# Optimization experiments

Measured on AMD Instinct MI355X. Metric: run time of the kernel, lower is better.

The kernel has to match this reference:

```python
import jax, jax.numpy as jnp
import numpy as np

H = W = 20  # module hardcodes visual_feature_map_h/w = 20
STAGES = 6
IN_POINTS = 36
HID = 256
B = 1024


def grid_sample_bilinear_border(fm, grid):
    """PyTorch-equivalent grid_sample, mode='bilinear', padding_mode='border',
    align_corners=False. fm: (B,C,H,W); grid: (B,P,2) in [-1,1] (x,y order).
    Returns (B,C,P)."""
    b, c, h, w = fm.shape
    # unnormalize (align_corners=False), then border-clip the coordinate
    x = jnp.clip((grid[..., 0] + 1.0) * w * 0.5 - 0.5, 0.0, w - 1.0)  # (B,P)
    y = jnp.clip((grid[..., 1] + 1.0) * h * 0.5 - 0.5, 0.0, h - 1.0)
    x0f = jnp.floor(x); y0f = jnp.floor(y)
    wx = (x - x0f)[:, None, :]  # (B,1,P)
    wy = (y - y0f)[:, None, :]
    x0 = x0f.astype(jnp.int32); y0 = y0f.astype(jnp.int32)
    x1 = jnp.minimum(x0 + 1, w - 1); y1 = jnp.minimum(y0 + 1, h - 1)
    fmf = fm.reshape(b, c, h * w)

    def gather(yi, xi):
        idx = (yi * w + xi)[:, None, :]  # (B,1,P)
        return jnp.take_along_axis(fmf, jnp.broadcast_to(idx, (b, c, idx.shape[-1])), axis=2)

    v00 = gather(y0, x0); v01 = gather(y0, x1)
    v10 = gather(y1, x0); v11 = gather(y1, x1)
    return (v00 * (1 - wx) * (1 - wy) + v01 * wx * (1 - wy)
            + v10 * (1 - wx) * wy + v11 * wx * wy)


def setup_inputs() -> dict:
    key = jax.random.key(0)
    ks = jax.random.split(key, 16)
    s = 0.02  # small param scale so sampled points stay mostly in-grid
    return {
        "sampling_query": jax.random.normal(ks[0], (B, HID), jnp.float32),
        "reference_point": jax.random.uniform(ks[1], (B, 2), jnp.float32),
        "feature_map": jax.random.normal(ks[2], (B, HID, H * W), jnp.float32),
        "pos": jax.random.normal(ks[3], (B, HID, H * W), jnp.float32),
        "offset_W": jax.random.normal(ks[4], (STAGES, IN_POINTS * 2, HID), jnp.float32) * s,
        "offset_b": jax.random.uniform(ks[5], (STAGES, IN_POINTS * 2), jnp.float32) - 0.5,
        "up_W1": jax.random.normal(ks[6], (STAGES, HID, 2 * HID), jnp.float32) * s,
        "up_b1": jax.random.normal(ks[7], (STAGES, HID), jnp.float32) * s,
        "up_W2": jax.random.normal(ks[8], (STAGES, HID, HID), jnp.float32) * s,
        "up_b2": jax.random.normal(ks[9], (STAGES, HID), jnp.float32) * s,
        "bbox_W1": jax.random.normal(ks[10], (HID, HID), jnp.float32) * s,
        "bbox_b1": jax.random.normal(ks[11], (HID,), jnp.float32) * s,
        "bbox_W2": jax.random.normal(ks[12], (HID, HID), jnp.float32) * s,
        "bbox_b2": jax.random.normal(ks[13], (HID,), jnp.float32) * s,
        "bbox_W3": jax.random.normal(ks[14], (4, HID), jnp.float32) * s,
        "bbox_b3": jax.random.normal(ks[15], (4,), jnp.float32) * s,
    }


def reference(sampling_query, reference_point, feature_map, pos,
              offset_W, offset_b, up_W1, up_b1, up_W2, up_b2,
              bbox_W1, bbox_b1, bbox_W2, bbox_b2, bbox_W3, bbox_b3):
    bs = sampling_query.shape[0]
    fm = feature_map.reshape(bs, HID, H, W)
    pm = pos.reshape(bs, HID, H, W)
    q = sampling_query
    for s in range(STAGES):  # fixed small stage count -> Python loop ok
        # offset generator: Linear(hidden -> in_points*2)
        xy = (q @ offset_W[s].T + offset_b[s]).reshape(bs, IN_POINTS, 2)
        pts = xy + reference_point[:, None, :]          # (B,P,2) in [0,1]
        grid = 2.0 * pts - 1.0                          # -> [-1,1]
        sampled = grid_sample_bilinear_border(fm, grid)  # (B,C,P)
        pe = grid_sample_bilinear_border(pm, grid)       # (B,C,P)
        fused = (sampled + pe).mean(axis=-1)             # (B,C) pooled over points
        # update_sampling_queries[s]: MLP(2*hidden -> hidden -> hidden)
        cat = jnp.concatenate([fused, q], axis=1)        # (B,2C)
        hdd = jax.nn.relu(cat @ up_W1[s].T + up_b1[s])
        q = hdd @ up_W2[s].T + up_b2[s]
    # bbox_embed: 3-layer MLP, relu on first two, sigmoid box
    hx = jax.nn.relu(q @ bbox_W1.T + bbox_b1)
    hx = jax.nn.relu(hx @ bbox_W2.T + bbox_b2)
    pred_box = jax.nn.sigmoid(hx @ bbox_W3.T + bbox_b3)  # (B,4)
    return pred_box
```

## Files before the change

kernel.cpp:

```cpp
#include <hip/hip_runtime.h>
#include <hip/hip_bf16.h>

#define B_SZ   1024
#define HIDN   256
#define NSTAGE 6
#define NPTS   36
#define HGT    20
#define WID    20
#define HW     400
#define MB     4
#define NTHR   1024

static __device__ __forceinline__ unsigned int f2bf(float x) {
    unsigned int u = __float_as_uint(x);
    u += 0x7FFFu + ((u >> 16) & 1u);
    return u >> 16;
}
static __device__ __forceinline__ float bf2f(unsigned short h) {
    return __uint_as_float((unsigned int)h << 16);
}

__global__ __launch_bounds__(512) void prepass_kernel(
    const float* __restrict__ fm, const float* __restrict__ pos,
    unsigned short* __restrict__ fmp)
{
    const int b  = blockIdx.y;
    const int ct = blockIdx.x;
    __shared__ unsigned short tile[HW * 65];
    const int t = threadIdx.x;

    const size_t gbase = ((size_t)b * HIDN + ct * 64) * HW;
    for (int i = t; i < 6400; i += 512) {
        const int c  = i / 100;
        const int k4 = i - c * 100;
        const float4 a = *(const float4*)(fm  + gbase + 4 * (size_t)i);
        const float4 p = *(const float4*)(pos + gbase + 4 * (size_t)i);
        tile[(4 * k4 + 0) * 65 + c] = (unsigned short)f2bf(a.x + p.x);
        tile[(4 * k4 + 1) * 65 + c] = (unsigned short)f2bf(a.y + p.y);
        tile[(4 * k4 + 2) * 65 + c] = (unsigned short)f2bf(a.z + p.z);
        tile[(4 * k4 + 3) * 65 + c] = (unsigned short)f2bf(a.w + p.w);
    }
    __syncthreads();

    const int u2 = t & 31;
    const int h0 = t >> 5;
    uint* outp = (uint*)(fmp + (((size_t)b * 4 + ct) * HW) * 64);
    for (int hw = h0; hw < HW; hw += 16) {
        const unsigned int lo = tile[hw * 65 + 2 * u2 + 0];
        const unsigned int hi = tile[hw * 65 + 2 * u2 + 1];
        outp[(size_t)hw * 32 + u2] = lo | (hi << 16);
    }
}

template <int K, int O, int ACT>
__device__ __forceinline__ void gemm_v3(
    const float* __restrict__ W, const float* __restrict__ bias,
    const float* __restrict__ i0, const float* __restrict__ i1,
    const float* __restrict__ i2, const float* __restrict__ i3,
    float* __restrict__ o0, float* __restrict__ o1,
    float* __restrict__ o2, float* __restrict__ o3,
    int kp, int og)
{
    const float4* p0 = (const float4*)i0;
    const float4* p1 = (const float4*)i1;
    const float4* p2 = (const float4*)i2;
    const float4* p3 = (const float4*)i3;
    #pragma unroll
    for (int pass = 0; pass < (O + 127) / 128; ++pass) {
        const int o = pass * 128 + og;
        float a0 = 0.f, a1 = 0.f, a2 = 0.f, a3 = 0.f;
        if (o < O) {
            const float4* wr = (const float4*)(W + (size_t)o * K);
            #pragma unroll 4
            for (int jj = 0; jj < K / 32; ++jj) {
                const int j = kp + 8 * jj;
                const float4 w  = wr[j];
                const float4 v0 = p0[j];
                const float4 v1 = p1[j];
                const float4 v2 = p2[j];
                const float4 v3 = p3[j];
                a0 += w.x * v0.x + w.y * v0.y + w.z * v0.z + w.w * v0.w;
                a1 += w.x * v1.x + w.y * v1.y + w.z * v1.z + w.w * v1.w;
                a2 += w.x * v2.x + w.y * v2.y + w.z * v2.z + w.w * v2.w;
                a3 += w.x * v3.x + w.y * v3.y + w.z * v3.z + w.w * v3.w;
            }
        }
        a0 += __shfl_xor(a0, 1); a0 += __shfl_xor(a0, 2); a0 += __shfl_xor(a0, 4);
        a1 += __shfl_xor(a1, 1); a1 += __shfl_xor(a1, 2); a1 += __shfl_xor(a1, 4);
        a2 += __shfl_xor(a2, 1); a2 += __shfl_xor(a2, 2); a2 += __shfl_xor(a2, 4);
        a3 += __shfl_xor(a3, 1); a3 += __shfl_xor(a3, 2); a3 += __shfl_xor(a3, 4);
        if (kp == 0 && o < O) {
            const float bz = bias[o];
            float r0 = a0 + bz, r1 = a1 + bz, r2 = a2 + bz, r3 = a3 + bz;
            if (ACT == 1) {
                r0 = fmaxf(r0, 0.f); r1 = fmaxf(r1, 0.f);
                r2 = fmaxf(r2, 0.f); r3 = fmaxf(r3, 0.f);
            }
            if (ACT == 2) {
                r0 = 1.f / (1.f + expf(-r0)); r1 = 1.f / (1.f + expf(-r1));
                r2 = 1.f / (1.f + expf(-r2)); r3 = 1.f / (1.f + expf(-r3));
            }
            o0[o] = r0; o1[o] = r1; o2[o] = r2; o3[o] = r3;
        }
    }
}

__global__ __launch_bounds__(NTHR) void mdetr5_kernel(
    const float* __restrict__ q_in,  const float* __restrict__ refpt,
    const unsigned short* __restrict__ fmp,
    const float* __restrict__ offW,  const float* __restrict__ offB,
    const float* __restrict__ uW1,   const float* __restrict__ uB1,
    const float* __restrict__ uW2,   const float* __restrict__ uB2,
    const float* __restrict__ bW1,   const float* __restrict__ bb1,
    const float* __restrict__ bW2,   const float* __restrict__ bb2,
    const float* __restrict__ bW3,   const float* __restrict__ bb3,
    float* __restrict__ out)
{
    const int b0 = blockIdx.x * MB;
    const int t  = threadIdx.x;
    const int kp = t & 7;
    const int og = t >> 3;

    __shared__ __attribute__((aligned(16))) float cat_s[MB][2 * HIDN];
    __shared__ __attribute__((aligned(16))) float hdd_s[MB][HIDN];
    __shared__ __attribute__((aligned(16))) float xy_s[MB][80];
    __shared__ __attribute__((aligned(16))) float wgt_s[MB][144];
    __shared__ __attribute__((aligned(16))) int   off_s[MB][144];

    {
        const int m = t >> 8, c = t & 255;
        cat_s[m][HIDN + c] = q_in[(size_t)(b0 + m) * HIDN + c];
    }

    for (int s = 0; s < NSTAGE; ++s) {
        __syncthreads();
        gemm_v3<HIDN, NPTS * 2, 0>(
            offW + (size_t)s * NPTS * 2 * HIDN, offB + s * NPTS * 2,
            cat_s[0] + HIDN, cat_s[1] + HIDN, cat_s[2] + HIDN, cat_s[3] + HIDN,
            xy_s[0], xy_s[1], xy_s[2], xy_s[3], kp, og);
        __syncthreads();
        if (t < MB * NPTS) {
            const int m = t / NPTS, p = t % NPTS;
            const int bm = b0 + m;
            float px = xy_s[m][2 * p + 0] + refpt[2 * bm + 0];
            float py = xy_s[m][2 * p + 1] + refpt[2 * bm + 1];
            float x = fminf(fmaxf(px * (float)WID - 0.5f, 0.f), (float)(WID - 1));
            float y = fminf(fmaxf(py * (float)HGT - 0.5f, 0.f), (float)(HGT - 1));
            float x0f = floorf(x), y0f = floorf(y);
            float wx = x - x0f,   wy = y - y0f;
            int x0 = (int)x0f, y0 = (int)y0f;
            int x1 = min(x0 + 1, WID - 1), y1 = min(y0 + 1, HGT - 1);
            const float inv = 1.f / (float)NPTS;
            wgt_s[m][4 * p + 0] = (1.f - wx) * (1.f - wy) * inv;
            wgt_s[m][4 * p + 1] = wx * (1.f - wy) * inv;
            wgt_s[m][4 * p + 2] = (1.f - wx) * wy * inv;
            wgt_s[m][4 * p + 3] = wx * wy * inv;
            off_s[m][4 * p + 0] = (y0 * WID + x0) * 64;
            off_s[m][4 * p + 1] = (y0 * WID + x1) * 64;
            off_s[m][4 * p + 2] = (y1 * WID + x0) * 64;
            off_s[m][4 * p + 3] = (y1 * WID + x1) * 64;
        }
        __syncthreads();
        {
            const int m = t >> 8, c = t & 255;
            const unsigned short* base =
                fmp + (((size_t)(b0 + m) * 4 + (c >> 6)) * HW) * 64 + (c & 63);
            float acc = 0.f;
            #pragma unroll 6
            for (int p = 0; p < NPTS; ++p) {
                const int4   o4 = ((const int4*)off_s[m])[p];
                const float4 w4 = ((const float4*)wgt_s[m])[p];
                acc += w4.x * bf2f(base[o4.x]) + w4.y * bf2f(base[o4.y])
                     + w4.z * bf2f(base[o4.z]) + w4.w * bf2f(base[o4.w]);
            }
            cat_s[m][c] = acc;
        }
        __syncthreads();
        gemm_v3<2 * HIDN, HIDN, 1>(
            uW1 + (size_t)s * HIDN * 2 * HIDN, uB1 + s * HIDN,
            cat_s[0], cat_s[1], cat_s[2], cat_s[3],
            hdd_s[0], hdd_s[1], hdd_s[2], hdd_s[3], kp, og);
        __syncthreads();
        gemm_v3<HIDN, HIDN, 0>(
            uW2 + (size_t)s * HIDN * HIDN, uB2 + s * HIDN,
            hdd_s[0], hdd_s[1], hdd_s[2], hdd_s[3],
            cat_s[0] + HIDN, cat_s[1] + HIDN, cat_s[2] + HIDN, cat_s[3] + HIDN,
            kp, og);
    }
    __syncthreads();
    gemm_v3<HIDN, HIDN, 1>(bW1, bb1,
        cat_s[0] + HIDN, cat_s[1] + HIDN, cat_s[2] + HIDN, cat_s[3] + HIDN,
        hdd_s[0], hdd_s[1], hdd_s[2], hdd_s[3], kp, og);
    __syncthreads();
    gemm_v3<HIDN, HIDN, 1>(bW2, bb2,
        hdd_s[0], hdd_s[1], hdd_s[2], hdd_s[3],
        cat_s[0], cat_s[1], cat_s[2], cat_s[3], kp, og);
    __syncthreads();
    gemm_v3<HIDN, 4, 2>(bW3, bb3,
        cat_s[0], cat_s[1], cat_s[2], cat_s[3],
        out + (size_t)(b0 + 0) * 4, out + (size_t)(b0 + 1) * 4,
        out + (size_t)(b0 + 2) * 4, out + (size_t)(b0 + 3) * 4, kp, og);
}

__global__ __launch_bounds__(256) void mdetr_direct_kernel(
    const float* __restrict__ q_in,  const float* __restrict__ refpt,
    const float* __restrict__ fm,    const float* __restrict__ pos,
    const float* __restrict__ offW,  const float* __restrict__ offB,
    const float* __restrict__ uW1,   const float* __restrict__ uB1,
    const float* __restrict__ uW2,   const float* __restrict__ uB2,
    const float* __restrict__ bW1,   const float* __restrict__ bb1,
    const float* __restrict__ bW2,   const float* __restrict__ bb2,
    const float* __restrict__ bW3,   const float* __restrict__ bb3,
    float* __restrict__ out)
{
    const int b = blockIdx.x;
    const int t = threadIdx.x;
    __shared__ __attribute__((aligned(16))) float q_s[HIDN];
    __shared__ __attribute__((aligned(16))) float fused_s[HIDN];
    __shared__ __attribute__((aligned(16))) float hdd_s[HIDN];
    __shared__ float xy_s[NPTS * 2];
    __shared__ int   off_s[NPTS * 4];
    __shared__ float w_s[NPTS * 4];

    q_s[t] = q_in[(size_t)b * HIDN + t];
    const float rpx = refpt[2 * b + 0];
    const float rpy = refpt[2 * b + 1];

    for (int s = 0; s < NSTAGE; ++s) {
        __syncthreads();
        if (t < NPTS * 2) {
            const float4* wrow = (const float4*)(offW + ((size_t)s * 72 + t) * HIDN);
            const float4* q4   = (const float4*)q_s;
            float a0 = 0.f;
            #pragma unroll 8
            for (int k = 0; k < HIDN / 4; ++k) {
                float4 w4 = wrow[k]; float4 qq = q4[k];
                a0 += w4.x * qq.x + w4.y * qq.y + w4.z * qq.z + w4.w * qq.w;
            }
            xy_s[t] = offB[s * 72 + t] + a0;
        }
        __syncthreads();
        if (t < NPTS) {
            float px = xy_s[2 * t + 0] + rpx;
            float py = xy_s[2 * t + 1] + rpy;
            float x = fminf(fmaxf(px * (float)WID - 0.5f, 0.f), (float)(WID - 1));
            float y = fminf(fmaxf(py * (float)HGT - 0.5f, 0.f), (float)(HGT - 1));
            float x0f = floorf(x), y0f = floorf(y);
            float wx = x - x0f, wy = y - y0f;
            int x0 = (int)x0f, y0 = (int)y0f;
            int x1 = min(x0 + 1, WID - 1), y1 = min(y0 + 1, HGT - 1);
            const float inv = 1.f / (float)NPTS;
            w_s[4 * t + 0] = (1.f - wx) * (1.f - wy) * inv;
            w_s[4 * t + 1] = wx * (1.f - wy) * inv;
            w_s[4 * t + 2] = (1.f - wx) * wy * inv;
            w_s[4 * t + 3] = wx * wy * inv;
            off_s[4 * t + 0] = y0 * WID + x0;
            off_s[4 * t + 1] = y0 * WID + x1;
            off_s[4 * t + 2] = y1 * WID + x0;
            off_s[4 * t + 3] = y1 * WID + x1;
        }
        __syncthreads();
        {
            float acc = 0.f;
            const float* basef = fm  + ((size_t)b * HIDN + t) * HW;
            const float* basep = pos + ((size_t)b * HIDN + t) * HW;
            #pragma unroll 6
            for (int p = 0; p < NPTS; ++p)
                for (int k = 0; k < 4; ++k) {
                    int idx = off_s[4 * p + k];
                    acc += w_s[4 * p + k] * (basef[idx] + basep[idx]);
                }
            fused_s[t] = acc;
        }
        __syncthreads();
        {
            const float4* w1 = (const float4*)(uW1 + ((size_t)s * HIDN + t) * (2 * HIDN));
            const float4* f4 = (const float4*)fused_s;
            const float4* q4 = (const float4*)q_s;
            float a0 = 0.f;
            #pragma unroll 8
            for (int k = 0; k < HIDN / 4; ++k) {
                float4 w4 = w1[k]; float4 c4 = f4[k];
                a0 += w4.x * c4.x + w4.y * c4.y + w4.z * c4.z + w4.w * c4.w;
            }
            #pragma unroll 8
            for (int k = 0; k < HIDN / 4; ++k) {
                float4 w4 = w1[HIDN / 4 + k]; float4 c4 = q4[k];
                a0 += w4.x * c4.x + w4.y * c4.y + w4.z * c4.z + w4.w * c4.w;
            }
            hdd_s[t] = fmaxf(uB1[s * HIDN + t] + a0, 0.f);
        }
        __syncthreads();
        {
            const float4* w2 = (const float4*)(uW2 + ((size_t)s * HIDN + t) * HIDN);
            const float4* h4 = (const float4*)hdd_s;
            float a0 = 0.f;
            #pragma unroll 8
            for (int k = 0; k < HIDN / 4; ++k) {
                float4 w4 = w2[k]; float4 c4 = h4[k];
                a0 += w4.x * c4.x + w4.y * c4.y + w4.z * c4.z + w4.w * c4.w;
            }
            q_s[t] = uB2[s * HIDN + t] + a0;
        }
    }
    __syncthreads();
    {
        const float4* w = (const float4*)(bW1 + (size_t)t * HIDN);
        const float4* q4 = (const float4*)q_s;
        float a0 = 0.f;
        #pragma unroll 8
        for (int k = 0; k < HIDN / 4; ++k) {
            float4 w4 = w[k]; float4 c4 = q4[k];
            a0 += w4.x * c4.x + w4.y * c4.y + w4.z * c4.z + w4.w * c4.w;
        }
        hdd_s[t] = fmaxf(bb1[t] + a0, 0.f);
    }
    __syncthreads();
    {
        const float4* w = (const float4*)(bW2 + (size_t)t * HIDN);
        const float4* h4 = (const float4*)hdd_s;
        float a0 = 0.f;
        #pragma unroll 8
        for (int k = 0; k < HIDN / 4; ++k) {
            float4 w4 = w[k]; float4 c4 = h4[k];
            a0 += w4.x * c4.x + w4.y * c4.y + w4.z * c4.z + w4.w * c4.w;
        }
        fused_s[t] = fmaxf(bb2[t] + a0, 0.f);
    }
    __syncthreads();
    if (t < 4) {
        const float* w = bW3 + (size_t)t * HIDN;
        float h = bb3[t];
        #pragma unroll 16
        for (int k = 0; k < HIDN; ++k) h += w[k] * fused_s[k];
        out[(size_t)b * 4 + t] = 1.f / (1.f + expf(-h));
    }
}

extern "C" void kernel_launch(void* const* d_in, const int* in_sizes, int n_in,
                              void* d_out, int out_size, void* d_ws, size_t ws_size,
                              hipStream_t stream)
{
    const float* q    = (const float*)d_in[0];
    const float* rp   = (const float*)d_in[1];
    const float* fm   = (const float*)d_in[2];
    const float* pos  = (const float*)d_in[3];
    const float* offW = (const float*)d_in[4];
    const float* offB = (const float*)d_in[5];
    const float* uW1  = (const float*)d_in[6];
    const float* uB1  = (const float*)d_in[7];
    const float* uW2  = (const float*)d_in[8];
    const float* uB2  = (const float*)d_in[9];
    const float* bW1  = (const float*)d_in[10];
    const float* bb1  = (const float*)d_in[11];
    const float* bW2  = (const float*)d_in[12];
    const float* bb2  = (const float*)d_in[13];
    const float* bW3  = (const float*)d_in[14];
    const float* bb3  = (const float*)d_in[15];
    float* out = (float*)d_out;

    const size_t need = (size_t)B_SZ * HW * HIDN * sizeof(unsigned short);
    if (ws_size >= need) {
        unsigned short* fmp = (unsigned short*)d_ws;
        prepass_kernel<<<dim3(HIDN / 64, B_SZ), 512, 0, stream>>>(fm, pos, fmp);
        mdetr5_kernel<<<B_SZ / MB, NTHR, 0, stream>>>(
            q, rp, fmp, offW, offB, uW1, uB1, uW2, uB2,
            bW1, bb1, bW2, bb2, bW3, bb3, out);
    } else {
        mdetr_direct_kernel<<<B_SZ, 256, 0, stream>>>(
            q, rp, fm, pos, offW, offB, uW1, uB1, uW2, uB2,
            bW1, bb1, bW2, bb2, bW3, bb3, out);
    }
}
```

Baseline: 352.4 us.

## Convert MLP weights to bf16 in a prepass and retune feature prepass

Adds a small kernel that converts all large MLP weight matrices to bf16 in the workspace, and a new GEMM routine that reads bf16 weight pairs and expands them to fp32 in registers. This halves the weight bytes each of the 256 blocks streams per stage. The feature-map prepass also moves to 640 threads with a fixed, partially unrolled loop that issues two float4 load pairs per iteration. It adds one extra launch and a larger workspace requirement, and bf16 weights introduce rounding error.

```diff
diff --git a/kernel.cpp b/kernel.cpp
--- a/kernel.cpp
+++ b/kernel.cpp
@@ -11,6 +11,13 @@
 #define MB     4
 #define NTHR   1024
 
+#define W_OFFW   0
+#define W_UW1    110592
+#define W_UW2    897024
+#define W_BW1    1290240
+#define W_BW2    1355776
+#define W_TOTAL  1421312
+
 static __device__ __forceinline__ unsigned int f2bf(float x) {
     unsigned int u = __float_as_uint(x);
     u += 0x7FFFu + ((u >> 16) & 1u);
@@ -19,8 +26,30 @@
 static __device__ __forceinline__ float bf2f(unsigned short h) {
     return __uint_as_float((unsigned int)h << 16);
 }
-
-__global__ __launch_bounds__(512) void prepass_kernel(
+static __device__ __forceinline__ float bflo(unsigned int u) {
+    return __uint_as_float(u << 16);
+}
+static __device__ __forceinline__ float bfhi(unsigned int u) {
+    return __uint_as_float(u & 0xFFFF0000u);
+}
+
+__global__ __launch_bounds__(256) void wconv_kernel(
+    const float* __restrict__ offW, const float* __restrict__ uW1,
+    const float* __restrict__ uW2,  const float* __restrict__ bW1,
+    const float* __restrict__ bW2,  unsigned short* __restrict__ dst)
+{
+    int i = blockIdx.x * 256 + threadIdx.x;
+    if (i >= W_TOTAL) return;
+    float v;
+    if (i < W_UW1)       v = offW[i - W_OFFW];
+    else if (i < W_UW2)  v = uW1[i - W_UW1];
+    else if (i < W_BW1)  v = uW2[i - W_UW2];
+    else if (i < W_BW2)  v = bW1[i - W_BW1];
+    else                 v = bW2[i - W_BW2];
+    dst[i] = (unsigned short)f2bf(v);
+}
+
+__global__ __launch_bounds__(640) void prepass_kernel(
     const float* __restrict__ fm, const float* __restrict__ pos,
     unsigned short* __restrict__ fmp)
 {
@@ -30,22 +59,33 @@
     const int t = threadIdx.x;
 
     const size_t gbase = ((size_t)b * HIDN + ct * 64) * HW;
-    for (int i = t; i < 6400; i += 512) {
-        const int c  = i / 100;
-        const int k4 = i - c * 100;
-        const float4 a = *(const float4*)(fm  + gbase + 4 * (size_t)i);
-        const float4 p = *(const float4*)(pos + gbase + 4 * (size_t)i);
-        tile[(4 * k4 + 0) * 65 + c] = (unsigned short)f2bf(a.x + p.x);
-        tile[(4 * k4 + 1) * 65 + c] = (unsigned short)f2bf(a.y + p.y);
-        tile[(4 * k4 + 2) * 65 + c] = (unsigned short)f2bf(a.z + p.z);
-        tile[(4 * k4 + 3) * 65 + c] = (unsigned short)f2bf(a.w + p.w);
+    #pragma unroll 1
+    for (int k = 0; k < 5; ++k) {
+        const int i0 = t + (2 * k) * 640;
+        const int i1 = i0 + 640;
+        const float4 a0 = *(const float4*)(fm  + gbase + 4 * (size_t)i0);
+        const float4 q0 = *(const float4*)(pos + gbase + 4 * (size_t)i0);
+        const float4 a1 = *(const float4*)(fm  + gbase + 4 * (size_t)i1);
+        const float4 q1 = *(const float4*)(pos + gbase + 4 * (size_t)i1);
+        const int c0 = i0 / 100, k40 = i0 - c0 * 100;
+        const int c1 = i1 / 100, k41 = i1 - c1 * 100;
+        tile[(4 * k40 + 0) * 65 + c0] = (unsigned short)f2bf(a0.x + q0.x);
+        tile[(4 * k40 + 1) * 65 + c0] = (unsigned short)f2bf(a0.y + q0.y);
+        tile[(4 * k40 + 2) * 65 + c0] = (unsigned short)f2bf(a0.z + q0.z);
+        tile[(4 * k40 + 3) * 65 + c0] = (unsigned short)f2bf(a0.w + q0.w);
+        tile[(4 * k41 + 0) * 65 + c1] = (unsigned short)f2bf(a1.x + q1.x);
+        tile[(4 * k41 + 1) * 65 + c1] = (unsigned short)f2bf(a1.y + q1.y);
+        tile[(4 * k41 + 2) * 65 + c1] = (unsigned short)f2bf(a1.z + q1.z);
+        tile[(4 * k41 + 3) * 65 + c1] = (unsigned short)f2bf(a1.w + q1.w);
     }
     __syncthreads();
 
     const int u2 = t & 31;
     const int h0 = t >> 5;
     uint* outp = (uint*)(fmp + (((size_t)b * 4 + ct) * HW) * 64);
-    for (int hw = h0; hw < HW; hw += 16) {
+    #pragma unroll
+    for (int w = 0; w < 20; ++w) {
+        const int hw = h0 + 20 * w;
         const unsigned int lo = tile[hw * 65 + 2 * u2 + 0];
         const unsigned int hi = tile[hw * 65 + 2 * u2 + 1];
         outp[(size_t)hw * 32 + u2] = lo | (hi << 16);
@@ -105,14 +145,69 @@
     }
 }
 
-__global__ __launch_bounds__(NTHR) void mdetr5_kernel(
+template <int K, int O, int ACT>
+__device__ __forceinline__ void gemm_bf(
+    const unsigned short* __restrict__ W, const float* __restrict__ bias,
+    const float* __restrict__ i0, const float* __restrict__ i1,
+    const float* __restrict__ i2, const float* __restrict__ i3,
+    float* __restrict__ o0, float* __restrict__ o1,
+    float* __restrict__ o2, float* __restrict__ o3,
+    int kp, int og)
+{
+    const float4* p0 = (const float4*)i0;
+    const float4* p1 = (const float4*)i1;
+    const float4* p2 = (const float4*)i2;
+    const float4* p3 = (const float4*)i3;
+    #pragma unroll
+    for (int pass = 0; pass < (O + 127) / 128; ++pass) {
+        const int o = pass * 128 + og;
+        float a0 = 0.f, a1 = 0.f, a2 = 0.f, a3 = 0.f;
+        if (o < O) {
+            const uint2* wr = (const uint2*)(W + (size_t)o * K);
+            #pragma unroll 4
+            for (int jj = 0; jj < K / 32; ++jj) {
+                const int j = kp + 8 * jj;
+                const uint2 wq = wr[j];
+                const float w0 = bflo(wq.x), w1 = bfhi(wq.x);
+                const float w2 = bflo(wq.y), w3 = bfhi(wq.y);
+                const float4 v0 = p0[j];
+                const float4 v1 = p1[j];
+                const float4 v2 = p2[j];
+                const float4 v3 = p3[j];
+                a0 += w0 * v0.x + w1 * v0.y + w2 * v0.z + w3 * v0.w;
+                a1 += w0 * v1.x + w1 * v1.y + w2 * v1.z + w3 * v1.w;
+                a2 += w0 * v2.x + w1 * v2.y + w2 * v2.z + w3 * v2.w;
+                a3 += w0 * v3.x + w1 * v3.y + w2 * v3.z + w3 * v3.w;
+            }
+        }
+        a0 += __shfl_xor(a0, 1); a0 += __shfl_xor(a0, 2); a0 += __shfl_xor(a0, 4);
+        a1 += __shfl_xor(a1, 1); a1 += __shfl_xor(a1, 2); a1 += __shfl_xor(a1, 4);
+        a2 += __shfl_xor(a2, 1); a2 += __shfl_xor(a2, 2); a2 += __shfl_xor(a2, 4);
+        a3 += __shfl_xor(a3, 1); a3 += __shfl_xor(a3, 2); a3 += __shfl_xor(a3, 4);
+        if (kp == 0 && o < O) {
+            const float bz = bias[o];
+            float r0 = a0 + bz, r1 = a1 + bz, r2 = a2 + bz, r3 = a3 + bz;
+            if (ACT == 1) {
+                r0 = fmaxf(r0, 0.f); r1 = fmaxf(r1, 0.f);
+                r2 = fmaxf(r2, 0.f); r3 = fmaxf(r3, 0.f);
+            }
+            if (ACT == 2) {
+                r0 = 1.f / (1.f + expf(-r0)); r1 = 1.f / (1.f + expf(-r1));
+                r2 = 1.f / (1.f + expf(-r2)); r3 = 1.f / (1.f + expf(-r3));
+            }
+            o0[o] = r0; o1[o] = r1; o2[o] = r2; o3[o] = r3;
+        }
+    }
+}
+
+__global__ __launch_bounds__(NTHR) void mdetr6_kernel(
     const float* __restrict__ q_in,  const float* __restrict__ refpt,
     const unsigned short* __restrict__ fmp,
-    const float* __restrict__ offW,  const float* __restrict__ offB,
-    const float* __restrict__ uW1,   const float* __restrict__ uB1,
-    const float* __restrict__ uW2,   const float* __restrict__ uB2,
-    const float* __restrict__ bW1,   const float* __restrict__ bb1,
-    const float* __restrict__ bW2,   const float* __restrict__ bb2,
+    const unsigned short* __restrict__ offWb, const float* __restrict__ offB,
+    const unsigned short* __restrict__ uW1b,  const float* __restrict__ uB1,
+    const unsigned short* __restrict__ uW2b,  const float* __restrict__ uB2,
+    const unsigned short* __restrict__ bW1b,  const float* __restrict__ bb1,
+    const unsigned short* __restrict__ bW2b,  const float* __restrict__ bb2,
     const float* __restrict__ bW3,   const float* __restrict__ bb3,
     float* __restrict__ out)
 {
@@ -134,8 +229,8 @@
 
     for (int s = 0; s < NSTAGE; ++s) {
         __syncthreads();
-        gemm_v3<HIDN, NPTS * 2, 0>(
-            offW + (size_t)s * NPTS * 2 * HIDN, offB + s * NPTS * 2,
+        gemm_bf<HIDN, NPTS * 2, 0>(
+            offWb + (size_t)s * NPTS * 2 * HIDN, offB + s * NPTS * 2,
             cat_s[0] + HIDN, cat_s[1] + HIDN, cat_s[2] + HIDN, cat_s[3] + HIDN,
             xy_s[0], xy_s[1], xy_s[2], xy_s[3], kp, og);
         __syncthreads();
@@ -176,23 +271,23 @@
             cat_s[m][c] = acc;
         }
         __syncthreads();
-        gemm_v3<2 * HIDN, HIDN, 1>(
-            uW1 + (size_t)s * HIDN * 2 * HIDN, uB1 + s * HIDN,
+        gemm_bf<2 * HIDN, HIDN, 1>(
+            uW1b + (size_t)s * HIDN * 2 * HIDN, uB1 + s * HIDN,
             cat_s[0], cat_s[1], cat_s[2], cat_s[3],
             hdd_s[0], hdd_s[1], hdd_s[2], hdd_s[3], kp, og);
         __syncthreads();
-        gemm_v3<HIDN, HIDN, 0>(
-            uW2 + (size_t)s * HIDN * HIDN, uB2 + s * HIDN,
+        gemm_bf<HIDN, HIDN, 0>(
+            uW2b + (size_t)s * HIDN * HIDN, uB2 + s * HIDN,
             hdd_s[0], hdd_s[1], hdd_s[2], hdd_s[3],
             cat_s[0] + HIDN, cat_s[1] + HIDN, cat_s[2] + HIDN, cat_s[3] + HIDN,
             kp, og);
     }
     __syncthreads();
-    gemm_v3<HIDN, HIDN, 1>(bW1, bb1,
+    gemm_bf<HIDN, HIDN, 1>(bW1b, bb1,
         cat_s[0] + HIDN, cat_s[1] + HIDN, cat_s[2] + HIDN, cat_s[3] + HIDN,
         hdd_s[0], hdd_s[1], hdd_s[2], hdd_s[3], kp, og);
     __syncthreads();
-    gemm_v3<HIDN, HIDN, 1>(bW2, bb2,
+    gemm_bf<HIDN, HIDN, 1>(bW2b, bb2,
         hdd_s[0], hdd_s[1], hdd_s[2], hdd_s[3],
         cat_s[0], cat_s[1], cat_s[2], cat_s[3], kp, og);
     __syncthreads();
@@ -359,13 +454,17 @@
     const float* bb3  = (const float*)d_in[15];
     float* out = (float*)d_out;
 
-    const size_t need = (size_t)B_SZ * HW * HIDN * sizeof(unsigned short);
+    const size_t fmp_elems = (size_t)B_SZ * HW * HIDN;
+    const size_t need = (fmp_elems + W_TOTAL) * sizeof(unsigned short);
     if (ws_size >= need) {
         unsigned short* fmp = (unsigned short*)d_ws;
-        prepass_kernel<<<dim3(HIDN / 64, B_SZ), 512, 0, stream>>>(fm, pos, fmp);
-        mdetr5_kernel<<<B_SZ / MB, NTHR, 0, stream>>>(
-            q, rp, fmp, offW, offB, uW1, uB1, uW2, uB2,
-            bW1, bb1, bW2, bb2, bW3, bb3, out);
+        unsigned short* wbf = fmp + fmp_elems;
+        wconv_kernel<<<W_TOTAL / 256, 256, 0, stream>>>(offW, uW1, uW2, bW1, bW2, wbf);
+        prepass_kernel<<<dim3(4, B_SZ), 640, 0, stream>>>(fm, pos, fmp);
+        mdetr6_kernel<<<B_SZ / MB, NTHR, 0, stream>>>(
+            q, rp, fmp,
+            wbf + W_OFFW, offB, wbf + W_UW1, uB1, wbf + W_UW2, uB2,
+            wbf + W_BW1, bb1, wbf + W_BW2, bb2, bW3, bb3, out);
     } else {
         mdetr_direct_kernel<<<B_SZ, 256, 0, stream>>>(
             q, rp, fm, pos, offW, offB, uW1, uB1, uW2, uB2,
```

Result: no change. 350.0 us, median of 2 (-0.7%).
